# Performance work log

Hardware: AMD Instinct MI355X
Metric: run time of the kernel (lower is better)

Reference implementation:

```python
import jax, jax.numpy as jnp
import numpy as np

N, P, Q, T, J, B, H = 262144, 64, 64, 2048, 512, 8, 64


def setup_inputs() -> dict:
    key = jax.random.key(0)
    ks = jax.random.split(key, 11)
    sH = 1.0 / np.sqrt(H).astype(np.float32)
    return {
        "idx": jax.random.randint(ks[0], (B,), 0, J),
        "seg_ids": jnp.sort(jax.random.randint(ks[1], (N,), 0, T)),
        "K": jax.random.normal(ks[2], (N, P), jnp.float32) * 0.1,
        "V": jax.random.normal(ks[3], (N, Q), jnp.float32),
        "S": jax.random.normal(ks[4], (P, J), jnp.float32) * 0.1,
        "W_ih": jax.random.normal(ks[5], (3 * H, Q), jnp.float32) * sH,
        "W_hh": jax.random.normal(ks[6], (3 * H, H), jnp.float32) * sH,
        "b_ih": jax.random.normal(ks[7], (3 * H,), jnp.float32) * sH,
        "b_hh": jax.random.normal(ks[8], (3 * H,), jnp.float32) * sH,
        "w_out": jax.random.normal(ks[9], (1, H), jnp.float32) * sH,
        "b_out": jax.random.normal(ks[10], (1,), jnp.float32) * sH,
    }


def reference(idx, seg_ids, K, V, S, W_ih, W_hh, b_ih, b_hh, w_out, b_out):
    # W[:, b] = K @ S[:, idx[b]]  -> [N, B]
    w = K @ S[:, idx]
    # ragged per-segment softmax over the N axis (segments = date windows)
    m = jax.ops.segment_max(w, seg_ids, num_segments=T)          # [T, B]
    e = jnp.exp(w - m[seg_ids])                                  # [N, B]
    denom = jax.ops.segment_sum(e, seg_ids, num_segments=T)     # [T, B]
    alpha = e / denom[seg_ids]                                   # [N, B]
    # weighted aggregation of V rows per segment: M[t, b] = sum_u alpha_u * V_u
    M = jax.ops.segment_sum(alpha[:, :, None] * V[:, None, :],
                            seg_ids, num_segments=T)             # [T, B, Q]
    X = jnp.transpose(M, (1, 0, 2))                              # [B, T, Q]

    # PyTorch GRU (gate order r,z,n). Faithful to the original bug: GRU was
    # built without batch_first=True, so axis 0 (B) is time, axis 1 (T) is batch.
    def step(h, x_t):  # x_t: [T, Q], h: [T, H]
        gi = x_t @ W_ih.T + b_ih                                 # [T, 3H]
        gh = h @ W_hh.T + b_hh                                   # [T, 3H]
        i_r, i_z, i_n = jnp.split(gi, 3, axis=1)
        h_r, h_z, h_n = jnp.split(gh, 3, axis=1)
        r = jax.nn.sigmoid(i_r + h_r)
        z = jax.nn.sigmoid(i_z + h_z)
        n = jnp.tanh(i_n + r * h_n)
        h_new = (1.0 - z) * n + z * h
        return h_new, h_new

    h0 = jnp.zeros((T, H), X.dtype)
    _, hs = jax.lax.scan(step, h0, X)                            # [B, T, H]
    preds = hs @ w_out.T + b_out                                 # [B, T, 1]
    return preds
```

## Files before the change

### kernel.cpp

```cpp
#include <hip/hip_runtime.h>
#include <math.h>

#define NN 262144
#define PP 64
#define QQ 64
#define TT 2048
#define JJ 512
#define BB 8
#define HH 64

__device__ __forceinline__ float lane_bcast(float v, int l) {
  return __int_as_float(__builtin_amdgcn_readlane(__float_as_int(v), l));
}

__global__ __launch_bounds__(256) void k_w(const float* __restrict__ Kmat,
                                           const int* __restrict__ idx,
                                           const float* __restrict__ S,
                                           float* __restrict__ ew) {
  __shared__ __align__(16) float s_lds[BB * PP];
  int tid = threadIdx.x;
  for (int i = tid; i < BB * PP; i += 256) {
    int p = i >> 3, b = i & 7;
    s_lds[b * PP + p] = S[p * JJ + idx[b]];
  }
  __syncthreads();
  int n = blockIdx.x * 64 + (tid >> 2);
  int sub = tid & 3;
  const float4* Kp = reinterpret_cast<const float4*>(Kmat + (size_t)n * PP + sub * 16);
  float4 kq[4];
#pragma unroll
  for (int j = 0; j < 4; ++j) kq[j] = Kp[j];
  float acc[8];
#pragma unroll
  for (int b = 0; b < 8; ++b) acc[b] = 0.f;
#pragma unroll
  for (int j4 = 0; j4 < 4; ++j4) {
    float4 kk = kq[j4];
#pragma unroll
    for (int b = 0; b < 8; ++b) {
      const float4 sv = *reinterpret_cast<const float4*>(&s_lds[b * PP + sub * 16 + j4 * 4]);
      acc[b] += kk.x * sv.x + kk.y * sv.y + kk.z * sv.z + kk.w * sv.w;
    }
  }
#pragma unroll
  for (int b = 0; b < 8; ++b) {
    acc[b] += __shfl_xor(acc[b], 1);
    acc[b] += __shfl_xor(acc[b], 2);
  }
  float ox = (sub == 0) ? acc[0] : (sub == 1) ? acc[2] : (sub == 2) ? acc[4] : acc[6];
  float oy = (sub == 0) ? acc[1] : (sub == 1) ? acc[3] : (sub == 2) ? acc[5] : acc[7];
  reinterpret_cast<float2*>(ew + (size_t)n * 8)[sub] =
      make_float2(__expf(ox), __expf(oy));
}

__global__ __launch_bounds__(256) void k_seg2(const float* __restrict__ ew,
                                              const float* __restrict__ V,
                                              const int* __restrict__ seg_ids,
                                              float* __restrict__ M) {
  __shared__ __align__(16) float accred[4][8][64];
  __shared__ float reds[4][8];
  __shared__ int bounds[2];
  int tid = threadIdx.x;
  int t = blockIdx.x;
  if (tid < 2) {
    int target = t + tid;
    int lo = 0, hi = NN;
    while (lo < hi) {
      int mid = (lo + hi) >> 1;
      if (seg_ids[mid] < target) lo = mid + 1; else hi = mid;
    }
    bounds[tid] = lo;
  }
  __syncthreads();
  int s = bounds[0], e = bounds[1];
  int lane = tid & 63, j = tid >> 6;
  int len = e - s;
  int chunk = (len + 3) >> 2;
  int b0 = s + j * chunk;
  int b1 = b0 + chunk; if (b1 > e) b1 = e;
  int slen = (b1 > b0) ? (b1 - b0) : 0;
  int rsub = lane >> 4;
  int qg = lane & 15;

  float4 acc[8];
#pragma unroll
  for (int b = 0; b < 8; ++b) acc[b] = make_float4(0.f, 0.f, 0.f, 0.f);
  float4 selo = make_float4(0.f, 0.f, 0.f, 0.f);
  float4 sehi = make_float4(0.f, 0.f, 0.f, 0.f);

#define PROC(RR)                                                                                           \
  {                                                                                                        \
    int r_ = (RR);                                                                                         \
    const float4* ewp_ = reinterpret_cast<const float4*>(ew + (size_t)r_ * 8);                             \
    float4 elo = ewp_[0], ehi = ewp_[1];                                                                   \
    float4 vv = reinterpret_cast<const float4*>(V + (size_t)r_ * QQ)[qg];                                  \
    selo.x += elo.x; selo.y += elo.y; selo.z += elo.z; selo.w += elo.w;                                    \
    sehi.x += ehi.x; sehi.y += ehi.y; sehi.z += ehi.z; sehi.w += ehi.w;                                    \
    acc[0].x += elo.x * vv.x; acc[0].y += elo.x * vv.y; acc[0].z += elo.x * vv.z; acc[0].w += elo.x * vv.w; \
    acc[1].x += elo.y * vv.x; acc[1].y += elo.y * vv.y; acc[1].z += elo.y * vv.z; acc[1].w += elo.y * vv.w; \
    acc[2].x += elo.z * vv.x; acc[2].y += elo.z * vv.y; acc[2].z += elo.z * vv.z; acc[2].w += elo.z * vv.w; \
    acc[3].x += elo.w * vv.x; acc[3].y += elo.w * vv.y; acc[3].z += elo.w * vv.z; acc[3].w += elo.w * vv.w; \
    acc[4].x += ehi.x * vv.x; acc[4].y += ehi.x * vv.y; acc[4].z += ehi.x * vv.z; acc[4].w += ehi.x * vv.w; \
    acc[5].x += ehi.y * vv.x; acc[5].y += ehi.y * vv.y; acc[5].z += ehi.y * vv.z; acc[5].w += ehi.y * vv.w; \
    acc[6].x += ehi.z * vv.x; acc[6].y += ehi.z * vv.y; acc[6].z += ehi.z * vv.z; acc[6].w += ehi.z * vv.w; \
    acc[7].x += ehi.w * vv.x; acc[7].y += ehi.w * vv.y; acc[7].z += ehi.w * vv.z; acc[7].w += ehi.w * vv.w; \
  }

  int nfull = slen >> 2, tail = slen & 3;
  int i = 0;
  for (; i + 2 <= nfull; i += 2) {
    PROC(b0 + i * 4 + rsub);
    PROC(b0 + (i + 1) * 4 + rsub);
  }
  if (i < nfull) PROC(b0 + i * 4 + rsub);
  if (tail && rsub < tail) PROC(b0 + nfull * 4 + rsub);
#undef PROC

#pragma unroll
  for (int b = 0; b < 8; ++b) {
    acc[b].x += __shfl_xor(acc[b].x, 16); acc[b].y += __shfl_xor(acc[b].y, 16);
    acc[b].z += __shfl_xor(acc[b].z, 16); acc[b].w += __shfl_xor(acc[b].w, 16);
    acc[b].x += __shfl_xor(acc[b].x, 32); acc[b].y += __shfl_xor(acc[b].y, 32);
    acc[b].z += __shfl_xor(acc[b].z, 32); acc[b].w += __shfl_xor(acc[b].w, 32);
  }
  selo.x += __shfl_xor(selo.x, 16); selo.y += __shfl_xor(selo.y, 16);
  selo.z += __shfl_xor(selo.z, 16); selo.w += __shfl_xor(selo.w, 16);
  sehi.x += __shfl_xor(sehi.x, 16); sehi.y += __shfl_xor(sehi.y, 16);
  sehi.z += __shfl_xor(sehi.z, 16); sehi.w += __shfl_xor(sehi.w, 16);
  selo.x += __shfl_xor(selo.x, 32); selo.y += __shfl_xor(selo.y, 32);
  selo.z += __shfl_xor(selo.z, 32); selo.w += __shfl_xor(selo.w, 32);
  sehi.x += __shfl_xor(sehi.x, 32); sehi.y += __shfl_xor(sehi.y, 32);
  sehi.z += __shfl_xor(sehi.z, 32); sehi.w += __shfl_xor(sehi.w, 32);

  if (rsub == 0) {
#pragma unroll
    for (int b = 0; b < 8; ++b)
      *reinterpret_cast<float4*>(&accred[j][b][qg * 4]) = acc[b];
    if (qg == 0) {
      reds[j][0] = selo.x; reds[j][1] = selo.y; reds[j][2] = selo.z; reds[j][3] = selo.w;
      reds[j][4] = sehi.x; reds[j][5] = sehi.y; reds[j][6] = sehi.z; reds[j][7] = sehi.w;
    }
  }
  __syncthreads();
  for (int o = tid; o < 512; o += 256) {
    int b = o >> 6, q = o & 63;
    float dd = reds[0][b] + reds[1][b] + reds[2][b] + reds[3][b];
    float inv = (dd > 0.f) ? 1.f / dd : 0.f;
    float sum = accred[0][b][q] + accred[1][b][q] + accred[2][b][q] + accred[3][b][q];
    M[(size_t)t * 512 + o] = sum * inv;
  }
}

__global__ __launch_bounds__(256) void k_gi(const float* __restrict__ M,
                                            const float* __restrict__ W_ih,
                                            const float* __restrict__ b_ih,
                                            float* __restrict__ GI) {
  __shared__ float Wt[64 * 193];
  int tid = threadIdx.x;
  for (int i = tid; i < 192 * 64; i += 256) {
    int g = i >> 6, k = i & 63;
    Wt[k * 193 + g] = W_ih[i];
  }
  __syncthreads();
  int lane = tid & 63, wv = tid >> 6;
  int row0 = blockIdx.x * 32 + wv * 8;
  float x[8];
#pragma unroll
  for (int rr = 0; rr < 8; ++rr) {
    int rho = row0 + rr;
    int b = rho >> 11, t = rho & 2047;
    x[rr] = M[((size_t)t * 8 + b) * 64 + lane];
  }
  float bi0 = b_ih[lane], bi1 = b_ih[64 + lane], bi2 = b_ih[128 + lane];
  float a0[8], a1[8], a2[8];
#pragma unroll
  for (int rr = 0; rr < 8; ++rr) { a0[rr] = bi0; a1[rr] = bi1; a2[rr] = bi2; }
#pragma unroll
  for (int k = 0; k < 64; ++k) {
    float w0 = Wt[k * 193 + lane];
    float w1 = Wt[k * 193 + 64 + lane];
    float w2 = Wt[k * 193 + 128 + lane];
#pragma unroll
    for (int rr = 0; rr < 8; ++rr) {
      float xk = lane_bcast(x[rr], k);
      a0[rr] += w0 * xk; a1[rr] += w1 * xk; a2[rr] += w2 * xk;
    }
  }
#pragma unroll
  for (int rr = 0; rr < 8; ++rr) {
    size_t rho = (size_t)row0 + rr;
    GI[rho * 192 + lane]       = a0[rr];
    GI[rho * 192 + 64 + lane]  = a1[rr];
    GI[rho * 192 + 128 + lane] = a2[rr];
  }
}

__global__ __launch_bounds__(256) void k_gru(const float* __restrict__ GI,
                                             const float* __restrict__ W_hh,
                                             const float* __restrict__ b_hh,
                                             const float* __restrict__ w_out,
                                             const float* __restrict__ b_out,
                                             float* __restrict__ preds) {
  __shared__ __align__(16) float Wl[192 * 68];
  int tid = threadIdx.x;
  for (int i = tid; i < 192 * 16; i += 256) {
    int g = i >> 4, c = i & 15;
    *reinterpret_cast<float4*>(&Wl[g * 68 + c * 4]) =
        *reinterpret_cast<const float4*>(W_hh + g * 64 + c * 4);
  }
  __syncthreads();
  int lane = tid & 63, wv = tid >> 6;
  int t = blockIdx.x * 4 + wv;
  float bh0 = b_hh[lane], bh1 = b_hh[64 + lane], bh2 = b_hh[128 + lane];
  float wo = w_out[lane];
  float bo = b_out[0];
  const float* w0base = &Wl[lane * 68];
  const float* w1base = &Wl[(64 + lane) * 68];
  const float* w2base = &Wl[(128 + lane) * 68];

  float gr[8], gz[8], gn[8];
#pragma unroll
  for (int b = 0; b < 8; ++b) {
    size_t base = ((size_t)b * TT + t) * 192;
    gr[b] = GI[base + lane];
    gz[b] = GI[base + 64 + lane];
    gn[b] = GI[base + 128 + lane];
  }

  float h;
  {
    float r = 1.f / (1.f + __expf(-(gr[0] + bh0)));
    float z = 1.f / (1.f + __expf(-(gz[0] + bh1)));
    float nv = tanhf(gn[0] + r * bh2);
    h = (1.f - z) * nv;
    float pv = h * wo;
#pragma unroll
    for (int off = 32; off; off >>= 1) pv += __shfl_xor(pv, off);
    if (lane == 0) preds[t] = pv + bo;
  }
#pragma unroll
  for (int b = 1; b < 8; ++b) {
    float ar = bh0, az = bh1, an = bh2;
#pragma unroll
    for (int c = 0; c < 16; ++c) {
      const float4 w0 = *reinterpret_cast<const float4*>(w0base + c * 4);
      const float4 w1 = *reinterpret_cast<const float4*>(w1base + c * 4);
      const float4 w2 = *reinterpret_cast<const float4*>(w2base + c * 4);
      float a0 = lane_bcast(h, c * 4 + 0), a1 = lane_bcast(h, c * 4 + 1);
      float a2 = lane_bcast(h, c * 4 + 2), a3 = lane_bcast(h, c * 4 + 3);
      ar += w0.x * a0 + w0.y * a1 + w0.z * a2 + w0.w * a3;
      az += w1.x * a0 + w1.y * a1 + w1.z * a2 + w1.w * a3;
      an += w2.x * a0 + w2.y * a1 + w2.z * a2 + w2.w * a3;
    }
    float r = 1.f / (1.f + __expf(-(gr[b] + ar)));
    float z = 1.f / (1.f + __expf(-(gz[b] + az)));
    float nv = tanhf(gn[b] + r * an);
    h = (1.f - z) * nv + z * h;
    float pv = h * wo;
#pragma unroll
    for (int off = 32; off; off >>= 1) pv += __shfl_xor(pv, off);
    if (lane == 0) preds[(size_t)b * TT + t] = pv + bo;
  }
}

extern "C" void kernel_launch(void* const* d_in, const int* in_sizes, int n_in,
                              void* d_out, int out_size, void* d_ws, size_t ws_size,
                              hipStream_t stream) {
  const int*   idx     = (const int*)d_in[0];
  const int*   seg_ids = (const int*)d_in[1];
  const float* Kmat    = (const float*)d_in[2];
  const float* V       = (const float*)d_in[3];
  const float* S       = (const float*)d_in[4];
  const float* W_ih    = (const float*)d_in[5];
  const float* W_hh    = (const float*)d_in[6];
  const float* b_ih    = (const float*)d_in[7];
  const float* b_hh    = (const float*)d_in[8];
  const float* w_out   = (const float*)d_in[9];
  const float* b_out   = (const float*)d_in[10];
  float* out = (float*)d_out;

  char* ws = (char*)d_ws;
  float* ew = (float*)(ws + 0);
  float* M  = (float*)(ws + 8388608);
  float* GI = (float*)(ws + 12582912);

  hipLaunchKernelGGL(k_w, dim3(NN / 64), dim3(256), 0, stream, Kmat, idx, S, ew);
  hipLaunchKernelGGL(k_seg2, dim3(TT), dim3(256), 0, stream, ew, V, seg_ids, M);
  hipLaunchKernelGGL(k_gi, dim3(512), dim3(256), 0, stream, M, W_ih, b_ih, GI);
  hipLaunchKernelGGL(k_gru, dim3(512), dim3(256), 0, stream, GI, W_hh, b_hh, w_out, b_out, out);
}
```

Measured before the change: 78.41 us.

## Fuse score/exp kernel with segment aggregation using atomics into zeroed accumulators

Merges the K·S score+exp kernel with the per-segment weighted V aggregation so exp weights stay in LDS instead of round-tripping an 8 MB buffer. Each block processes 64 contiguous rows and flushes partial per-segment sums and denominators via global atomicAdd, with normalization deferred to k_gi. This removes the binary search and the intermediate ew traffic but adds a memset, many atomics at segment boundaries, and non-deterministic summation order.

```diff
diff --git a/kernel.cpp b/kernel.cpp
--- a/kernel.cpp
+++ b/kernel.cpp
@@ -13,72 +13,58 @@
   return __int_as_float(__builtin_amdgcn_readlane(__float_as_int(v), l));
 }
 
-__global__ __launch_bounds__(256) void k_w(const float* __restrict__ Kmat,
-                                           const int* __restrict__ idx,
-                                           const float* __restrict__ S,
-                                           float* __restrict__ ew) {
-  __shared__ __align__(16) float s_lds[BB * PP];
+__global__ __launch_bounds__(256) void k_fused(const float* __restrict__ Kmat,
+                                               const int* __restrict__ idx,
+                                               const float* __restrict__ S,
+                                               const float* __restrict__ V,
+                                               const int* __restrict__ seg_ids,
+                                               float* __restrict__ Macc,
+                                               float* __restrict__ seacc) {
+  __shared__ __align__(16) float s_cols[BB * PP];
+  __shared__ __align__(16) float ew_lds[64 * 8];
+  __shared__ int seg_lds[64];
   int tid = threadIdx.x;
+  int n0 = blockIdx.x * 64;
   for (int i = tid; i < BB * PP; i += 256) {
     int p = i >> 3, b = i & 7;
-    s_lds[b * PP + p] = S[p * JJ + idx[b]];
-  }
+    s_cols[b * PP + p] = S[p * JJ + idx[b]];
+  }
+  if (tid < 64) seg_lds[tid] = seg_ids[n0 + tid];
   __syncthreads();
-  int n = blockIdx.x * 64 + (tid >> 2);
-  int sub = tid & 3;
-  const float4* Kp = reinterpret_cast<const float4*>(Kmat + (size_t)n * PP + sub * 16);
-  float4 kq[4];
-#pragma unroll
-  for (int j = 0; j < 4; ++j) kq[j] = Kp[j];
-  float acc[8];
-#pragma unroll
-  for (int b = 0; b < 8; ++b) acc[b] = 0.f;
-#pragma unroll
-  for (int j4 = 0; j4 < 4; ++j4) {
-    float4 kk = kq[j4];
+
+  {
+    int n = n0 + (tid >> 2);
+    int sub = tid & 3;
+    const float4* Kp = reinterpret_cast<const float4*>(Kmat + (size_t)n * PP + sub * 16);
+    float4 kq[4];
+#pragma unroll
+    for (int j = 0; j < 4; ++j) kq[j] = Kp[j];
+    float acc[8];
+#pragma unroll
+    for (int b = 0; b < 8; ++b) acc[b] = 0.f;
+#pragma unroll
+    for (int j4 = 0; j4 < 4; ++j4) {
+      float4 kk = kq[j4];
+#pragma unroll
+      for (int b = 0; b < 8; ++b) {
+        const float4 sv = *reinterpret_cast<const float4*>(&s_cols[b * PP + sub * 16 + j4 * 4]);
+        acc[b] += kk.x * sv.x + kk.y * sv.y + kk.z * sv.z + kk.w * sv.w;
+      }
+    }
 #pragma unroll
     for (int b = 0; b < 8; ++b) {
-      const float4 sv = *reinterpret_cast<const float4*>(&s_lds[b * PP + sub * 16 + j4 * 4]);
-      acc[b] += kk.x * sv.x + kk.y * sv.y + kk.z * sv.z + kk.w * sv.w;
-    }
-  }
-#pragma unroll
-  for (int b = 0; b < 8; ++b) {
-    acc[b] += __shfl_xor(acc[b], 1);
-    acc[b] += __shfl_xor(acc[b], 2);
-  }
-  float ox = (sub == 0) ? acc[0] : (sub == 1) ? acc[2] : (sub == 2) ? acc[4] : acc[6];
-  float oy = (sub == 0) ? acc[1] : (sub == 1) ? acc[3] : (sub == 2) ? acc[5] : acc[7];
-  reinterpret_cast<float2*>(ew + (size_t)n * 8)[sub] =
-      make_float2(__expf(ox), __expf(oy));
-}
-
-__global__ __launch_bounds__(256) void k_seg2(const float* __restrict__ ew,
-                                              const float* __restrict__ V,
-                                              const int* __restrict__ seg_ids,
-                                              float* __restrict__ M) {
-  __shared__ __align__(16) float accred[4][8][64];
-  __shared__ float reds[4][8];
-  __shared__ int bounds[2];
-  int tid = threadIdx.x;
-  int t = blockIdx.x;
-  if (tid < 2) {
-    int target = t + tid;
-    int lo = 0, hi = NN;
-    while (lo < hi) {
-      int mid = (lo + hi) >> 1;
-      if (seg_ids[mid] < target) lo = mid + 1; else hi = mid;
-    }
-    bounds[tid] = lo;
+      acc[b] += __shfl_xor(acc[b], 1);
+      acc[b] += __shfl_xor(acc[b], 2);
+    }
+    float ox = (sub == 0) ? acc[0] : (sub == 1) ? acc[2] : (sub == 2) ? acc[4] : acc[6];
+    float oy = (sub == 0) ? acc[1] : (sub == 1) ? acc[3] : (sub == 2) ? acc[5] : acc[7];
+    *reinterpret_cast<float2*>(&ew_lds[(tid >> 2) * 8 + 2 * sub]) =
+        make_float2(__expf(ox), __expf(oy));
   }
   __syncthreads();
-  int s = bounds[0], e = bounds[1];
-  int lane = tid & 63, j = tid >> 6;
-  int len = e - s;
-  int chunk = (len + 3) >> 2;
-  int b0 = s + j * chunk;
-  int b1 = b0 + chunk; if (b1 > e) b1 = e;
-  int slen = (b1 > b0) ? (b1 - b0) : 0;
+
+  int lane = tid & 63, wv = tid >> 6;
+  int wr0 = wv * 16;
   int rsub = lane >> 4;
   int qg = lane & 15;
 
@@ -87,13 +73,17 @@
   for (int b = 0; b < 8; ++b) acc[b] = make_float4(0.f, 0.f, 0.f, 0.f);
   float4 selo = make_float4(0.f, 0.f, 0.f, 0.f);
   float4 sehi = make_float4(0.f, 0.f, 0.f, 0.f);
-
-#define PROC(RR)                                                                                           \
+  int cur_t = seg_lds[wr0];
+
+#define ACCUM(RL, PRED)                                                                                    \
   {                                                                                                        \
-    int r_ = (RR);                                                                                         \
-    const float4* ewp_ = reinterpret_cast<const float4*>(ew + (size_t)r_ * 8);                             \
-    float4 elo = ewp_[0], ehi = ewp_[1];                                                                   \
-    float4 vv = reinterpret_cast<const float4*>(V + (size_t)r_ * QQ)[qg];                                  \
+    int rl_ = (RL);                                                                                        \
+    float pr_ = (PRED);                                                                                    \
+    float4 elo = *reinterpret_cast<const float4*>(&ew_lds[rl_ * 8]);                                       \
+    float4 ehi = *reinterpret_cast<const float4*>(&ew_lds[rl_ * 8 + 4]);                                   \
+    elo.x *= pr_; elo.y *= pr_; elo.z *= pr_; elo.w *= pr_;                                                \
+    ehi.x *= pr_; ehi.y *= pr_; ehi.z *= pr_; ehi.w *= pr_;                                                \
+    float4 vv = reinterpret_cast<const float4*>(V + (size_t)(n0 + rl_) * QQ)[qg];                          \
     selo.x += elo.x; selo.y += elo.y; selo.z += elo.z; selo.w += elo.w;                                    \
     sehi.x += ehi.x; sehi.y += ehi.y; sehi.z += ehi.z; sehi.w += ehi.w;                                    \
     acc[0].x += elo.x * vv.x; acc[0].y += elo.x * vv.y; acc[0].z += elo.x * vv.z; acc[0].w += elo.x * vv.w; \
@@ -106,52 +96,73 @@
     acc[7].x += ehi.w * vv.x; acc[7].y += ehi.w * vv.y; acc[7].z += ehi.w * vv.z; acc[7].w += ehi.w * vv.w; \
   }
 
-  int nfull = slen >> 2, tail = slen & 3;
-  int i = 0;
-  for (; i + 2 <= nfull; i += 2) {
-    PROC(b0 + i * 4 + rsub);
-    PROC(b0 + (i + 1) * 4 + rsub);
-  }
-  if (i < nfull) PROC(b0 + i * 4 + rsub);
-  if (tail && rsub < tail) PROC(b0 + nfull * 4 + rsub);
-#undef PROC
-
-#pragma unroll
-  for (int b = 0; b < 8; ++b) {
-    acc[b].x += __shfl_xor(acc[b].x, 16); acc[b].y += __shfl_xor(acc[b].y, 16);
-    acc[b].z += __shfl_xor(acc[b].z, 16); acc[b].w += __shfl_xor(acc[b].w, 16);
-    acc[b].x += __shfl_xor(acc[b].x, 32); acc[b].y += __shfl_xor(acc[b].y, 32);
-    acc[b].z += __shfl_xor(acc[b].z, 32); acc[b].w += __shfl_xor(acc[b].w, 32);
-  }
-  selo.x += __shfl_xor(selo.x, 16); selo.y += __shfl_xor(selo.y, 16);
-  selo.z += __shfl_xor(selo.z, 16); selo.w += __shfl_xor(selo.w, 16);
-  sehi.x += __shfl_xor(sehi.x, 16); sehi.y += __shfl_xor(sehi.y, 16);
-  sehi.z += __shfl_xor(sehi.z, 16); sehi.w += __shfl_xor(sehi.w, 16);
-  selo.x += __shfl_xor(selo.x, 32); selo.y += __shfl_xor(selo.y, 32);
-  selo.z += __shfl_xor(selo.z, 32); selo.w += __shfl_xor(selo.w, 32);
-  sehi.x += __shfl_xor(sehi.x, 32); sehi.y += __shfl_xor(sehi.y, 32);
-  sehi.z += __shfl_xor(sehi.z, 32); sehi.w += __shfl_xor(sehi.w, 32);
-
-  if (rsub == 0) {
-#pragma unroll
-    for (int b = 0; b < 8; ++b)
-      *reinterpret_cast<float4*>(&accred[j][b][qg * 4]) = acc[b];
-    if (qg == 0) {
-      reds[j][0] = selo.x; reds[j][1] = selo.y; reds[j][2] = selo.z; reds[j][3] = selo.w;
-      reds[j][4] = sehi.x; reds[j][5] = sehi.y; reds[j][6] = sehi.z; reds[j][7] = sehi.w;
-    }
-  }
-  __syncthreads();
-  for (int o = tid; o < 512; o += 256) {
-    int b = o >> 6, q = o & 63;
-    float dd = reds[0][b] + reds[1][b] + reds[2][b] + reds[3][b];
-    float inv = (dd > 0.f) ? 1.f / dd : 0.f;
-    float sum = accred[0][b][q] + accred[1][b][q] + accred[2][b][q] + accred[3][b][q];
-    M[(size_t)t * 512 + o] = sum * inv;
-  }
-}
-
-__global__ __launch_bounds__(256) void k_gi(const float* __restrict__ M,
+#define FLUSH(TSEG)                                                                                        \
+  {                                                                                                        \
+    int t_ = (TSEG);                                                                                       \
+    _Pragma("unroll")                                                                                      \
+    for (int b = 0; b < 8; ++b) {                                                                          \
+      acc[b].x += __shfl_xor(acc[b].x, 16); acc[b].y += __shfl_xor(acc[b].y, 16);                          \
+      acc[b].z += __shfl_xor(acc[b].z, 16); acc[b].w += __shfl_xor(acc[b].w, 16);                          \
+      acc[b].x += __shfl_xor(acc[b].x, 32); acc[b].y += __shfl_xor(acc[b].y, 32);                          \
+      acc[b].z += __shfl_xor(acc[b].z, 32); acc[b].w += __shfl_xor(acc[b].w, 32);                          \
+    }                                                                                                      \
+    selo.x += __shfl_xor(selo.x, 16); selo.y += __shfl_xor(selo.y, 16);                                    \
+    selo.z += __shfl_xor(selo.z, 16); selo.w += __shfl_xor(selo.w, 16);                                    \
+    sehi.x += __shfl_xor(sehi.x, 16); sehi.y += __shfl_xor(sehi.y, 16);                                    \
+    sehi.z += __shfl_xor(sehi.z, 16); sehi.w += __shfl_xor(sehi.w, 16);                                    \
+    selo.x += __shfl_xor(selo.x, 32); selo.y += __shfl_xor(selo.y, 32);                                    \
+    selo.z += __shfl_xor(selo.z, 32); selo.w += __shfl_xor(selo.w, 32);                                    \
+    sehi.x += __shfl_xor(sehi.x, 32); sehi.y += __shfl_xor(sehi.y, 32);                                    \
+    sehi.z += __shfl_xor(sehi.z, 32); sehi.w += __shfl_xor(sehi.w, 32);                                    \
+    if (rsub == 0) {                                                                                       \
+      float* mp = Macc + (size_t)t_ * 512 + qg * 4;                                                        \
+      _Pragma("unroll")                                                                                    \
+      for (int b = 0; b < 8; ++b) {                                                                        \
+        atomicAdd(mp + b * 64 + 0, acc[b].x); atomicAdd(mp + b * 64 + 1, acc[b].y);                        \
+        atomicAdd(mp + b * 64 + 2, acc[b].z); atomicAdd(mp + b * 64 + 3, acc[b].w);                        \
+      }                                                                                                    \
+      if (qg == 0) {                                                                                       \
+        float* sp = seacc + (size_t)t_ * 8;                                                                \
+        atomicAdd(sp + 0, selo.x); atomicAdd(sp + 1, selo.y);                                              \
+        atomicAdd(sp + 2, selo.z); atomicAdd(sp + 3, selo.w);                                              \
+        atomicAdd(sp + 4, sehi.x); atomicAdd(sp + 5, sehi.y);                                              \
+        atomicAdd(sp + 6, sehi.z); atomicAdd(sp + 7, sehi.w);                                              \
+      }                                                                                                    \
+    }                                                                                                      \
+    _Pragma("unroll")                                                                                      \
+    for (int b = 0; b < 8; ++b) acc[b] = make_float4(0.f, 0.f, 0.f, 0.f);                                  \
+    selo = make_float4(0.f, 0.f, 0.f, 0.f);                                                                \
+    sehi = make_float4(0.f, 0.f, 0.f, 0.f);                                                                \
+  }
+
+#pragma unroll
+  for (int iq = 0; iq < 4; ++iq) {
+    int q0 = wr0 + iq * 4;
+    int rl = q0 + rsub;
+    int t0 = seg_lds[q0];
+    int t3 = seg_lds[q0 + 3];
+    if (t0 == t3 && t0 == cur_t) {
+      ACCUM(rl, 1.0f);
+    } else if (t0 == t3) {
+      FLUSH(cur_t);
+      cur_t = t0;
+      ACCUM(rl, 1.0f);
+    } else {
+#pragma unroll
+      for (int rr = 0; rr < 4; ++rr) {
+        int trr = seg_lds[q0 + rr];
+        if (trr != cur_t) { FLUSH(cur_t); cur_t = trr; }
+        ACCUM(rl, (rsub == rr) ? 1.0f : 0.0f);
+      }
+    }
+  }
+  FLUSH(cur_t);
+#undef ACCUM
+#undef FLUSH
+}
+
+__global__ __launch_bounds__(256) void k_gi(const float* __restrict__ Macc,
+                                            const float* __restrict__ seacc,
                                             const float* __restrict__ W_ih,
                                             const float* __restrict__ b_ih,
                                             float* __restrict__ GI) {
@@ -169,7 +180,9 @@
   for (int rr = 0; rr < 8; ++rr) {
     int rho = row0 + rr;
     int b = rho >> 11, t = rho & 2047;
-    x[rr] = M[((size_t)t * 8 + b) * 64 + lane];
+    float dd = seacc[t * 8 + b];
+    float inv = (dd > 0.f) ? 1.f / dd : 0.f;
+    x[rr] = Macc[((size_t)t * 8 + b) * 64 + lane] * inv;
   }
   float bi0 = b_ih[lane], bi1 = b_ih[64 + lane], bi2 = b_ih[128 + lane];
   float a0[8], a1[8], a2[8];
@@ -280,12 +293,13 @@
   float* out = (float*)d_out;
 
   char* ws = (char*)d_ws;
-  float* ew = (float*)(ws + 0);
-  float* M  = (float*)(ws + 8388608);
-  float* GI = (float*)(ws + 12582912);
-
-  hipLaunchKernelGGL(k_w, dim3(NN / 64), dim3(256), 0, stream, Kmat, idx, S, ew);
-  hipLaunchKernelGGL(k_seg2, dim3(TT), dim3(256), 0, stream, ew, V, seg_ids, M);
-  hipLaunchKernelGGL(k_gi, dim3(512), dim3(256), 0, stream, M, W_ih, b_ih, GI);
+  float* Macc  = (float*)(ws + 0);
+  float* seacc = (float*)(ws + 4194304);
+  float* GI    = (float*)(ws + 4259840);
+
+  hipMemsetAsync(ws, 0, 4259840, stream);
+  hipLaunchKernelGGL(k_fused, dim3(NN / 64), dim3(256), 0, stream,
+                     Kmat, idx, S, V, seg_ids, Macc, seacc);
+  hipLaunchKernelGGL(k_gi, dim3(512), dim3(256), 0, stream, Macc, seacc, W_ih, b_ih, GI);
   hipLaunchKernelGGL(k_gru, dim3(512), dim3(256), 0, stream, GI, W_hh, b_hh, w_out, b_out, out);
 }
```

Result: slower. 197.4 us (+151.7%).
